# Performance work log

Hardware: AMD Instinct MI355X
Metric: run time of the kernel (lower is better)

Reference implementation:

```python
import jax, jax.numpy as jnp
import numpy as np

D_MODEL = 1024
NUM_HEADS = 16
D_K = D_MODEL // NUM_HEADS
SCALE = float(np.sqrt(D_K))


def setup_inputs() -> dict:
    key = jax.random.key(0)
    ks = jax.random.split(key, 9)
    B, S = 4, 2048
    x = jax.random.normal(ks[0], (B, S, D_MODEL), dtype=jnp.float32)
    init = 1.0 / np.sqrt(D_MODEL)
    def lin(kw, kb):
        W = jax.random.uniform(kw, (D_MODEL, D_MODEL), jnp.float32, -init, init)
        b = jax.random.uniform(kb, (D_MODEL,), jnp.float32, -init, init)
        return W, b
    Wq, bq = lin(ks[1], ks[2])
    Wk, bk = lin(ks[3], ks[4])
    Wv, bv = lin(ks[5], ks[6])
    Wo, bo = lin(ks[7], ks[8])
    return {"x": x, "Wq": Wq, "bq": bq, "Wk": Wk, "bk": bk,
            "Wv": Wv, "bv": bv, "Wo": Wo, "bo": bo}


def reference(x, Wq, bq, Wk, bk, Wv, bv, Wo, bo):
    B, S, _ = x.shape
    # projections (torch Linear: y = x @ W.T + b)
    q = x @ Wq.T + bq
    k = x @ Wk.T + bk
    v = x @ Wv.T + bv
    # [B, H, S, d_k]
    q = q.reshape(B, S, NUM_HEADS, D_K).transpose(0, 2, 1, 3)
    k = k.reshape(B, S, NUM_HEADS, D_K).transpose(0, 2, 1, 3)
    v = v.reshape(B, S, NUM_HEADS, D_K).transpose(0, 2, 1, 3)
    # explicit scores [B, H, S, S]
    scores = jnp.einsum('bhqd,bhkd->bhqk', q, k) / SCALE
    attn = jax.nn.softmax(scores, axis=-1)
    # dropout is identity in eval mode
    ctx = jnp.einsum('bhqk,bhkd->bhqd', attn, v)
    ctx = ctx.transpose(0, 2, 1, 3).reshape(B, S, D_MODEL)
    return ctx @ Wo.T + bo
```

## Files before the change

kernel.cpp:

```cpp
#include <hip/hip_runtime.h>
#include <stdint.h>


typedef __attribute__((ext_vector_type(8))) short short8;
typedef __attribute__((ext_vector_type(4))) float f32x4;
typedef __attribute__((ext_vector_type(16))) float f32x16;
typedef __attribute__((ext_vector_type(4))) unsigned int u32x4;
typedef __attribute__((ext_vector_type(4))) unsigned short us4;
typedef unsigned short ushort_t;
typedef unsigned int uint_t;

#define DMODEL 1024
#define SEQ 2048
#define NH 16
#define QSCALE 0.18033688011112043f

__device__ __forceinline__ ushort_t bfbits(float f) {
  uint32_t u = __float_as_uint(f);
  u = (u + 0x7fffu + ((u >> 16) & 1u)) >> 16;
  return (ushort_t)u;
}
__device__ __forceinline__ uint_t cvt_pk_bf16(float lo, float hi) {
  uint_t r;
  asm("v_cvt_pk_bf16_f32 %0, %1, %2" : "=v"(r) : "v"(lo), "v"(hi));
  return r;
}
__device__ __forceinline__ float exp2_hw(float x) {
  float r;
  asm("v_exp_f32 %0, %1" : "=v"(r) : "v"(x));
  return r;
}
__device__ __forceinline__ f32x16 mfma32(short8 a, short8 b, f32x16 c) {
  return __builtin_amdgcn_mfma_f32_32x32x16_bf16(a, b, c, 0, 0, 0);
}

typedef __attribute__((address_space(1))) void gvoid_t;
typedef __attribute__((address_space(3))) void lvoid_t;
__device__ __forceinline__ void gl_lds16(const void* gp, void* lp) {
  __builtin_amdgcn_global_load_lds((gvoid_t*)(uintptr_t)gp, (lvoid_t*)lp, 16, 0, 0);
}

__global__ __launch_bounds__(256) void cvt_bf16(const float* __restrict__ in,
                                                ushort_t* __restrict__ out) {
  int i = (int)(blockIdx.x * 256u + threadIdx.x) * 8;
  const float4* p = (const float4*)(in + i);
  float4 a = p[0], b = p[1];
  short8 o;
  o[0] = (short)bfbits(a.x); o[1] = (short)bfbits(a.y);
  o[2] = (short)bfbits(a.z); o[3] = (short)bfbits(a.w);
  o[4] = (short)bfbits(b.x); o[5] = (short)bfbits(b.y);
  o[6] = (short)bfbits(b.z); o[7] = (short)bfbits(b.w);
  *(short8*)(out + i) = o;
}

__global__ __launch_bounds__(256) void cvt4_bf16(const float* __restrict__ w0,
                                                 const float* __restrict__ w1,
                                                 const float* __restrict__ w2,
                                                 const float* __restrict__ w3,
                                                 ushort_t* __restrict__ out) {
  int which = (int)(blockIdx.x >> 9);
  const float* src = (which == 0) ? w0 : (which == 1) ? w1 : (which == 2) ? w2 : w3;
  int i = (int)(((blockIdx.x & 511) * 256u) + threadIdx.x) * 8;
  const float4* p = (const float4*)(src + i);
  float4 a = p[0], b = p[1];
  short8 o;
  o[0] = (short)bfbits(a.x); o[1] = (short)bfbits(a.y);
  o[2] = (short)bfbits(a.z); o[3] = (short)bfbits(a.w);
  o[4] = (short)bfbits(b.x); o[5] = (short)bfbits(b.y);
  o[6] = (short)bfbits(b.z); o[7] = (short)bfbits(b.w);
  *(short8*)(out + (size_t)which * 1048576 + i) = o;
}

#define EPI_QKV 0
#define EPI_OUT 1

template <int EPI>
__global__ __launch_bounds__(256) void gemm_bt(const ushort_t* __restrict__ A,
                                               const ushort_t* __restrict__ Bw,
                                               const float* __restrict__ b0,
                                               const float* __restrict__ b1,
                                               const float* __restrict__ b2,
                                               ushort_t* __restrict__ Qb,
                                               ushort_t* __restrict__ Kb,
                                               ushort_t* __restrict__ Vtb,
                                               float* __restrict__ Yf) {
  __shared__ alignas(16) ushort_t As[3][128 * 32];
  __shared__ alignas(16) ushort_t Bs[3][128 * 32];
  const int tid = threadIdx.x;
  const int lane = tid & 63, w = tid >> 6;
  const int g = lane >> 4, r16 = lane & 15;
  const int wr = w >> 1, wc = w & 1;

  int nwg = (int)(gridDim.x * gridDim.y);
  int flat = (int)(blockIdx.x + gridDim.x * blockIdx.y);
  int cpx = nwg >> 3;
  int sw = (flat & 7) * cpx + (flat >> 3);
  const int bm0 = (sw & 63) * 128;
  const int bn0 = (sw >> 6) * 128;

  f32x4 acc[4][4];
#pragma unroll
  for (int m = 0; m < 4; ++m)
#pragma unroll
    for (int n = 0; n < 4; ++n) acc[m][n] = (f32x4){0.f, 0.f, 0.f, 0.f};

  const int srow = tid >> 2;
  const int sc = (tid & 3) * 8;

  auto stage = [&](int bf, int k0) {
    char* AsB = (char*)As[bf];
    char* BsB = (char*)Bs[bf];
    gl_lds16(A + (size_t)(bm0 + srow) * DMODEL + k0 + sc, AsB + w * 1024);
    gl_lds16(A + (size_t)(bm0 + 64 + srow) * DMODEL + k0 + sc, AsB + w * 1024 + 4096);
    gl_lds16(Bw + (size_t)(bn0 + srow) * DMODEL + k0 + sc, BsB + w * 1024);
    gl_lds16(Bw + (size_t)(bn0 + 64 + srow) * DMODEL + k0 + sc, BsB + w * 1024 + 4096);
  };

  stage(0, 0);
  stage(1, 32);
  int buf = 0;
  for (int t = 0; t < 32; ++t) {
    if (t < 31)
      asm volatile("s_waitcnt vmcnt(4)\n\ts_barrier" ::: "memory");
    else
      asm volatile("s_waitcnt vmcnt(0)\n\ts_barrier" ::: "memory");
    if (t < 30) stage((t + 2) % 3, (t + 2) * 32);

    const char* AsB = (const char*)As[buf];
    const char* BsB = (const char*)Bs[buf];
    short8 af[4], bfr[4];
#pragma unroll
    for (int m = 0; m < 4; ++m)
      af[m] = *(const short8*)(AsB + (wr * 64 + m * 16 + r16) * 64 + g * 16);
#pragma unroll
    for (int n = 0; n < 4; ++n)
      bfr[n] = *(const short8*)(BsB + (wc * 64 + n * 16 + r16) * 64 + g * 16);
    __builtin_amdgcn_s_setprio(1);
#pragma unroll
    for (int m = 0; m < 4; ++m)
#pragma unroll
      for (int n = 0; n < 4; ++n)
        acc[m][n] = __builtin_amdgcn_mfma_f32_16x16x32_bf16(af[m], bfr[n], acc[m][n], 0, 0, 0);
    __builtin_amdgcn_s_setprio(0);
    buf = (buf == 2) ? 0 : buf + 1;
  }

  if (EPI == EPI_OUT) {
    float bv[4];
#pragma unroll
    for (int n = 0; n < 4; ++n) bv[n] = b0[bn0 + wc * 64 + n * 16 + r16];
#pragma unroll
    for (int m = 0; m < 4; ++m)
#pragma unroll
      for (int r = 0; r < 4; ++r) {
        int grow = bm0 + wr * 64 + m * 16 + 4 * g + r;
        float* orow = Yf + (size_t)grow * DMODEL + bn0 + wc * 64;
#pragma unroll
        for (int n = 0; n < 4; ++n) orow[n * 16 + r16] = acc[m][n][r] + bv[n];
      }
  } else {
    int mat = bn0 >> 10;
    const float* bias = (mat == 0) ? b0 : (mat == 1 ? b1 : b2);
    ushort_t* dQK = (mat == 0) ? Qb : Kb;
    int nc0 = bn0 & 1023;
    float scl = (mat == 0) ? QSCALE : 1.0f;
    float bv[4];
#pragma unroll
    for (int n = 0; n < 4; ++n) bv[n] = bias[nc0 + wc * 64 + n * 16 + r16];
    if (mat < 2) {
#pragma unroll
      for (int m = 0; m < 4; ++m)
#pragma unroll
        for (int r = 0; r < 4; ++r) {
          int grow = bm0 + wr * 64 + m * 16 + 4 * g + r;
          int b = grow >> 11, s = grow & 2047;
#pragma unroll
          for (int n = 0; n < 4; ++n) {
            int gcl = nc0 + wc * 64 + n * 16 + r16;
            int h = gcl >> 6, d = gcl & 63;
            dQK[((size_t)(b * NH + h) * SEQ + s) * 64 + d] = bfbits((acc[m][n][r] + bv[n]) * scl);
          }
        }
    } else {
#pragma unroll
      for (int m = 0; m < 4; ++m) {
        int grow0 = bm0 + wr * 64 + m * 16 + 4 * g;
        int b = grow0 >> 11, s0 = grow0 & 2047;
#pragma unroll
        for (int n = 0; n < 4; ++n) {
          int gcl = nc0 + wc * 64 + n * 16 + r16;
          int h = gcl >> 6, d = gcl & 63;
          us4 pk;
          pk[0] = bfbits(acc[m][n][0] + bv[n]);
          pk[1] = bfbits(acc[m][n][1] + bv[n]);
          pk[2] = bfbits(acc[m][n][2] + bv[n]);
          pk[3] = bfbits(acc[m][n][3] + bv[n]);
          *(us4*)(Vtb + ((size_t)(b * NH + h) * 64 + d) * SEQ + s0) = pk;
        }
      }
    }
  }
}

__global__ __launch_bounds__(512, 4) void attn_fwd(const ushort_t* __restrict__ Q,
                                                   const ushort_t* __restrict__ K,
                                                   const ushort_t* __restrict__ Vt,
                                                   ushort_t* __restrict__ ctx) {
  __shared__ alignas(16) ushort_t Ks[3][64 * 64];
  __shared__ alignas(16) ushort_t Vs[3][64 * 64];
  const int tid = threadIdx.x;
  const int lane = tid & 63, w = tid >> 6;
  const int q32 = lane & 31, h = lane >> 5;

  int flat = (int)(blockIdx.x + 8 * blockIdx.y);
  int sw = (flat & 7) * 64 + (flat >> 3);
  int bh = sw >> 3, q0 = (sw & 7) * 256;

  const ushort_t* Qp = Q + (size_t)bh * SEQ * 64;
  const ushort_t* Kp = K + (size_t)bh * SEQ * 64;
  const ushort_t* Vp = Vt + (size_t)bh * 64 * SEQ;

  short8 qf[4];
  {
    const ushort_t* qr = Qp + (size_t)(q0 + w * 32 + q32) * 64 + h * 8;
    qf[0] = *(const short8*)(qr);
    qf[1] = *(const short8*)(qr + 16);
    qf[2] = *(const short8*)(qr + 32);
    qf[3] = *(const short8*)(qr + 48);
  }

  f32x16 o0 = (f32x16)0.0f, o1 = (f32x16)0.0f, lacc = (f32x16)0.0f;
  short8 ones;
#pragma unroll
  for (int j = 0; j < 8; ++j) ones[j] = (short)0x3F80;

  const int swz = (q32 & 7) << 4;

  auto stage = [&](int bf, int kv0) {
    int row = tid >> 3;
    int cs = (tid & 7) ^ (row & 7);
    gl_lds16(Kp + (size_t)(kv0 + row) * 64 + cs * 8, (char*)Ks[bf] + w * 1024);
    gl_lds16(Vp + (size_t)row * SEQ + kv0 + cs * 8, (char*)Vs[bf] + w * 1024);
  };

  stage(0, 0);
  stage(1, 64);
  int buf = 0;
  for (int t = 0; t < 32; ++t) {
    if (t < 31)
      asm volatile("s_waitcnt vmcnt(2)\n\ts_barrier" ::: "memory");
    else
      asm volatile("s_waitcnt vmcnt(0)\n\ts_barrier" ::: "memory");
    if (t < 30) stage((t + 2) % 3, (t + 2) * 64);

    const char* kb0 = (const char*)Ks[buf] + q32 * 128;
    const char* kb1 = kb0 + 32 * 128;
    const char* vb0 = (const char*)Vs[buf] + q32 * 128;
    const char* vb1 = vb0 + 32 * 128;

    f32x16 s0 = (f32x16)0.0f, s1 = (f32x16)0.0f;
    __builtin_amdgcn_s_setprio(1);
#pragma unroll
    for (int c = 0; c < 4; ++c) {
      short8 kf0 = *(const short8*)(kb0 + ((32 * c + 16 * h) ^ swz));
      short8 kf1 = *(const short8*)(kb1 + ((32 * c + 16 * h) ^ swz));
      s0 = mfma32(kf0, qf[c], s0);
      s1 = mfma32(kf1, qf[c], s1);
    }
    __builtin_amdgcn_s_setprio(0);

#pragma unroll
    for (int j = 0; j < 16; ++j) {
      s0[j] = exp2_hw(s0[j]);
      s1[j] = exp2_hw(s1[j]);
    }

    uint_t pw[16];
#pragma unroll
    for (int i = 0; i < 8; ++i) {
      pw[i] = cvt_pk_bf16(s0[2 * i], s0[2 * i + 1]);
      pw[8 + i] = cvt_pk_bf16(s1[2 * i], s1[2 * i + 1]);
    }
#pragma unroll
    for (int c = 0; c < 4; ++c) {
      asm volatile("v_permlane32_swap_b32 %0, %1" : "+v"(pw[4 * c]), "+v"(pw[4 * c + 2]));
      asm volatile("v_permlane32_swap_b32 %0, %1" : "+v"(pw[4 * c + 1]), "+v"(pw[4 * c + 3]));
    }

    __builtin_amdgcn_s_setprio(1);
#pragma unroll
    for (int c = 0; c < 4; ++c) {
      u32x4 pk = {pw[4 * c], pw[4 * c + 1], pw[4 * c + 2], pw[4 * c + 3]};
      short8 pfc = __builtin_bit_cast(short8, pk);
      short8 vf0 = *(const short8*)(vb0 + ((32 * c + 16 * h) ^ swz));
      short8 vf1 = *(const short8*)(vb1 + ((32 * c + 16 * h) ^ swz));
      o0 = mfma32(vf0, pfc, o0);
      o1 = mfma32(vf1, pfc, o1);
      lacc = mfma32(ones, pfc, lacc);
    }
    __builtin_amdgcn_s_setprio(0);

    buf = (buf == 2) ? 0 : buf + 1;
  }

  float inv = 1.0f / lacc[0];
  int b = bh >> 4, hd = bh & 15;
  uint_t* crow = (uint_t*)(ctx + ((size_t)(b * SEQ + q0 + w * 32 + q32)) * DMODEL + hd * 64);
#pragma unroll
  for (int i = 0; i < 8; ++i) {
    int ui = (i & 1) + 4 * (i >> 1) + 2 * h;
    crow[ui] = cvt_pk_bf16(o0[2 * i] * inv, o0[2 * i + 1] * inv);
    crow[16 + ui] = cvt_pk_bf16(o1[2 * i] * inv, o1[2 * i + 1] * inv);
  }
}

extern "C" void kernel_launch(void* const* d_in, const int* in_sizes, int n_in,
                              void* d_out, int out_size, void* d_ws, size_t ws_size,
                              hipStream_t stream) {
  (void)in_sizes; (void)n_in; (void)out_size; (void)ws_size;
  const float* x  = (const float*)d_in[0];
  const float* Wq = (const float*)d_in[1];
  const float* bq = (const float*)d_in[2];
  const float* Wk = (const float*)d_in[3];
  const float* bk = (const float*)d_in[4];
  const float* Wv = (const float*)d_in[5];
  const float* bv = (const float*)d_in[6];
  const float* Wo = (const float*)d_in[7];
  const float* bo = (const float*)d_in[8];
  float* out = (float*)d_out;

  ushort_t* xb  = (ushort_t*)d_ws;
  ushort_t* w3  = xb + 8388608;
  ushort_t* wob = w3 + 3145728;
  ushort_t* Qb  = wob + 1048576;
  ushort_t* Kb  = Qb + 8388608;
  ushort_t* Vtb = Kb + 8388608;
  ushort_t* cx  = Vtb + 8388608;

  cvt_bf16<<<4096, 256, 0, stream>>>(x, xb);
  cvt4_bf16<<<2048, 256, 0, stream>>>(Wq, Wk, Wv, Wo, w3);

  gemm_bt<EPI_QKV><<<dim3(64, 24), 256, 0, stream>>>(xb, w3, bq, bk, bv, Qb, Kb, Vtb, nullptr);
  attn_fwd<<<dim3(8, 64), 512, 0, stream>>>(Qb, Kb, Vtb, cx);
  gemm_bt<EPI_OUT><<<dim3(64, 8), 256, 0, stream>>>(cx, wob, bo, nullptr, nullptr,
                                                    nullptr, nullptr, nullptr, out);
}
```

Baseline: 284.6 us.

## Swizzle GEMM LDS reads, remap tiles per XCD, compute softmax sum with VALU

The GEMM kernel now XOR-swizzles the 16-byte column chunks when staging A/B tiles into shared memory and when reading them back, to reduce LDS bank conflicts. Tile-to-workgroup mapping is rewritten per XCD so blocks on the same XCD share rows and columns of the operands for better L2 reuse. In attention, the row-sum of probabilities is no longer computed by an extra MFMA against a ones vector. It is instead accumulated with VALU adds on the fp32 exponentials plus a cross-half shuffle, which removes a third of the PV-phase MFMAs but adds scalar adds and sums unrounded rather than bf16-rounded values.

```diff
diff --git a/kernel.cpp b/kernel.cpp
--- a/kernel.cpp
+++ b/kernel.cpp
@@ -91,12 +91,16 @@
   const int g = lane >> 4, r16 = lane & 15;
   const int wr = w >> 1, wc = w & 1;
 
-  int nwg = (int)(gridDim.x * gridDim.y);
   int flat = (int)(blockIdx.x + gridDim.x * blockIdx.y);
-  int cpx = nwg >> 3;
-  int sw = (flat & 7) * cpx + (flat >> 3);
-  const int bm0 = (sw & 63) * 128;
-  const int bn0 = (sw >> 6) * 128;
+  int xcd = flat & 7, local = flat >> 3;
+  int bm0, bn0;
+  if (EPI == EPI_QKV) {
+    bm0 = ((xcd & 3) * 16 + (local & 15)) * 128;
+    bn0 = ((xcd >> 2) * 12 + (local >> 4)) * 128;
+  } else {
+    bm0 = (xcd * 8 + (local & 7)) * 128;
+    bn0 = (local >> 3) * 128;
+  }
 
   f32x4 acc[4][4];
 #pragma unroll
@@ -105,15 +109,16 @@
     for (int n = 0; n < 4; ++n) acc[m][n] = (f32x4){0.f, 0.f, 0.f, 0.f};
 
   const int srow = tid >> 2;
-  const int sc = (tid & 3) * 8;
+  const int scs = ((tid & 3) ^ ((tid >> 3) & 3)) * 8;
+  const int rsw = (r16 >> 1) & 3;
 
   auto stage = [&](int bf, int k0) {
     char* AsB = (char*)As[bf];
     char* BsB = (char*)Bs[bf];
-    gl_lds16(A + (size_t)(bm0 + srow) * DMODEL + k0 + sc, AsB + w * 1024);
-    gl_lds16(A + (size_t)(bm0 + 64 + srow) * DMODEL + k0 + sc, AsB + w * 1024 + 4096);
-    gl_lds16(Bw + (size_t)(bn0 + srow) * DMODEL + k0 + sc, BsB + w * 1024);
-    gl_lds16(Bw + (size_t)(bn0 + 64 + srow) * DMODEL + k0 + sc, BsB + w * 1024 + 4096);
+    gl_lds16(A + (size_t)(bm0 + srow) * DMODEL + k0 + scs, AsB + w * 1024);
+    gl_lds16(A + (size_t)(bm0 + 64 + srow) * DMODEL + k0 + scs, AsB + w * 1024 + 4096);
+    gl_lds16(Bw + (size_t)(bn0 + srow) * DMODEL + k0 + scs, BsB + w * 1024);
+    gl_lds16(Bw + (size_t)(bn0 + 64 + srow) * DMODEL + k0 + scs, BsB + w * 1024 + 4096);
   };
 
   stage(0, 0);
@@ -131,10 +136,10 @@
     short8 af[4], bfr[4];
 #pragma unroll
     for (int m = 0; m < 4; ++m)
-      af[m] = *(const short8*)(AsB + (wr * 64 + m * 16 + r16) * 64 + g * 16);
+      af[m] = *(const short8*)(AsB + (wr * 64 + m * 16 + r16) * 64 + (g ^ rsw) * 16);
 #pragma unroll
     for (int n = 0; n < 4; ++n)
-      bfr[n] = *(const short8*)(BsB + (wc * 64 + n * 16 + r16) * 64 + g * 16);
+      bfr[n] = *(const short8*)(BsB + (wc * 64 + n * 16 + r16) * 64 + (g ^ rsw) * 16);
     __builtin_amdgcn_s_setprio(1);
 #pragma unroll
     for (int m = 0; m < 4; ++m)
@@ -229,10 +234,8 @@
     qf[3] = *(const short8*)(qr + 48);
   }
 
-  f32x16 o0 = (f32x16)0.0f, o1 = (f32x16)0.0f, lacc = (f32x16)0.0f;
-  short8 ones;
-#pragma unroll
-  for (int j = 0; j < 8; ++j) ones[j] = (short)0x3F80;
+  f32x16 o0 = (f32x16)0.0f, o1 = (f32x16)0.0f;
+  float l = 0.f;
 
   const int swz = (q32 & 7) << 4;
 
@@ -275,6 +278,15 @@
       s1[j] = exp2_hw(s1[j]);
     }
 
+    {
+      f32x16 ts = s0 + s1;
+      float a = (ts[0] + ts[1]) + (ts[2] + ts[3]);
+      float b = (ts[4] + ts[5]) + (ts[6] + ts[7]);
+      float c2 = (ts[8] + ts[9]) + (ts[10] + ts[11]);
+      float d = (ts[12] + ts[13]) + (ts[14] + ts[15]);
+      l += (a + b) + (c2 + d);
+    }
+
     uint_t pw[16];
 #pragma unroll
     for (int i = 0; i < 8; ++i) {
@@ -296,14 +308,14 @@
       short8 vf1 = *(const short8*)(vb1 + ((32 * c + 16 * h) ^ swz));
       o0 = mfma32(vf0, pfc, o0);
       o1 = mfma32(vf1, pfc, o1);
-      lacc = mfma32(ones, pfc, lacc);
     }
     __builtin_amdgcn_s_setprio(0);
 
     buf = (buf == 2) ? 0 : buf + 1;
   }
 
-  float inv = 1.0f / lacc[0];
+  float ltot = l + __shfl_xor(l, 32);
+  float inv = 1.0f / ltot;
   int b = bh >> 4, hd = bh & 15;
   uint_t* crow = (uint_t*)(ctx + ((size_t)(b * SEQ + q0 + w * 32 + q32)) * DMODEL + hd * 64);
 #pragma unroll
```

Measured after the change: 273.1 us. 1.04x faster.
